# Kernel tuning notes

Hardware: AMD Instinct MI355X
Metric: run time of the kernel (lower is better)

## Reference

```python
import jax, jax.numpy as jnp
import numpy as np

B, N, H, V = 8192, 12, 512, 256  # batch, n_columns, hidden_size, per-column vocab
LN_EPS = 1e-5


def setup_inputs() -> dict:
    key = jax.random.key(0)
    k0, k1, k2, k3 = jax.random.split(key, 4)
    return {
        "input_embedding": jax.random.normal(k0, (B, H), dtype=jnp.float32),
        "features": jax.random.randint(k1, (B, N), 0, V),  # one categorical id per column
        "emb_tables": jax.random.normal(k2, (N, V, H), dtype=jnp.float32) * 0.02,
        "ln_gamma": jnp.ones((2 * H,), dtype=jnp.float32),
        "ln_beta": jnp.zeros((2 * H,), dtype=jnp.float32),
        "pred_W": jax.random.normal(k3, (N, 2 * H, V), dtype=jnp.float32) * 0.02,
        "pred_b": jnp.zeros((N, V), dtype=jnp.float32),
    }


def reference(input_embedding, features, emb_tables, ln_gamma, ln_beta, pred_W, pred_b):
    n = features.shape[1]
    # per-column embedding lookup: emb[b, n] = emb_tables[n, features[b, n]]  -> [B, N, H]
    emb = emb_tables[jnp.arange(n)[None, :], features]
    # _make_masked_sums: triu(diagonal=1) mask summed over dim 1 == exclusive prefix sum
    # over the column axis: masked_sums[b, j] = sum_{i < j} emb[b, i]
    masked_sums = jnp.cumsum(emb, axis=1) - emb  # [B, N, H]
    ctx = jnp.broadcast_to(input_embedding[:, None, :], emb.shape)  # [B, N, H]
    x = jnp.concatenate([ctx, masked_sums], axis=-1)  # [B, N, 2H]
    # LayerNorm over last dim, then exact (erf) GELU as in torch nn.GELU default
    mu = jnp.mean(x, axis=-1, keepdims=True)
    var = jnp.mean(jnp.square(x - mu), axis=-1, keepdims=True)
    xn = (x - mu) * jax.lax.rsqrt(var + LN_EPS) * ln_gamma + ln_beta
    act = jax.nn.gelu(xn, approximate=False)
    # per-column predictor heads: logits[b, n, :] = act[b, n, :] @ pred_W[n] + pred_b[n]
    logits = jnp.einsum('bnh,nhv->bnv', act, pred_W) + pred_b
    return logits
```

## Files before the change

### kernel.cpp

```cpp
#include <hip/hip_runtime.h>
#include <stdint.h>

#define B_SZ 8192
#define N_F 12
#define H_DIM 512
#define K_DIM 1024
#define V_DIM 256

typedef __attribute__((ext_vector_type(8))) __bf16 bf16x8;
typedef __attribute__((ext_vector_type(4))) float f32x4;

__device__ inline float gelu_f(float x) {
  float t = 1.5957691216057308f * x * (1.0f + 0.044715f * x * x);
  return x / (1.0f + __expf(-t));
}

__device__ inline void gld_lds16(const void* g, void* l) {
  __builtin_amdgcn_global_load_lds(
      (const __attribute__((address_space(1))) void*)g,
      (__attribute__((address_space(3))) void*)l, 16, 0, 0);
}

__global__ __launch_bounds__(256, 8) void k_prep(
    const float* __restrict__ ie, const int* __restrict__ feat,
    const float* __restrict__ tab, const float* __restrict__ gam,
    const float* __restrict__ bet, __bf16* actA,
    float* __restrict__ stats) {
  const int lane = threadIdx.x & 63;
  const int b = blockIdx.x * 4 + (threadIdx.x >> 6);

  const float* cb = ie + (size_t)b * H_DIM + lane * 8;
  float4 c0 = *(const float4*)cb;
  float4 c1 = *(const float4*)(cb + 4);
  float s = c0.x + c0.y + c0.z + c0.w + c1.x + c1.y + c1.z + c1.w;
  float q = c0.x * c0.x + c0.y * c0.y + c0.z * c0.z + c0.w * c0.w +
            c1.x * c1.x + c1.y * c1.y + c1.z * c1.z + c1.w * c1.w;
#pragma unroll
  for (int o = 1; o < 64; o <<= 1) {
    s += __shfl_xor(s, o, 64);
    q += __shfl_xor(q, o, 64);
  }
  const float S1 = s, Q1 = q;

  const float4 g0 = *(const float4*)(gam + H_DIM + lane * 8);
  const float4 g1 = *(const float4*)(gam + H_DIM + lane * 8 + 4);
  const float4 e0 = *(const float4*)(bet + H_DIM + lane * 8);
  const float4 e1 = *(const float4*)(bet + H_DIM + lane * 8 + 4);

  float r[8];
#pragma unroll
  for (int i = 0; i < 8; ++i) r[i] = 0.f;

  const int sw = (lane & ~7) | ((lane & 7) ^ (b & 7));
  __bf16* arow = actA + (size_t)b * N_F * H_DIM + sw * 8;

  for (int n = 0; n < N_F; ++n) {
    s = 0.f; q = 0.f;
#pragma unroll
    for (int i = 0; i < 8; ++i) { s += r[i]; q += r[i] * r[i]; }
#pragma unroll
    for (int o = 1; o < 64; o <<= 1) {
      s += __shfl_xor(s, o, 64);
      q += __shfl_xor(q, o, 64);
    }
    const float mean = (S1 + s) * (1.0f / 1024.0f);
    const float var = (Q1 + q) * (1.0f / 1024.0f) - mean * mean;
    const float rs = rsqrtf(var + 1e-5f);
    if (lane == 0)
      *(float2*)(stats + ((size_t)b * N_F + n) * 2) = make_float2(mean, rs);

    float4 t0, t1;
    const bool have = (n < N_F - 1);
    if (have) {
      const int f = feat[b * N_F + n];
      const float* tr = tab + ((size_t)n * V_DIM + f) * H_DIM + lane * 8;
      t0 = *(const float4*)tr;
      t1 = *(const float4*)(tr + 4);
    }

    bf16x8 pk;
    pk[0] = (__bf16)gelu_f((r[0] - mean) * rs * g0.x + e0.x);
    pk[1] = (__bf16)gelu_f((r[1] - mean) * rs * g0.y + e0.y);
    pk[2] = (__bf16)gelu_f((r[2] - mean) * rs * g0.z + e0.z);
    pk[3] = (__bf16)gelu_f((r[3] - mean) * rs * g0.w + e0.w);
    pk[4] = (__bf16)gelu_f((r[4] - mean) * rs * g1.x + e1.x);
    pk[5] = (__bf16)gelu_f((r[5] - mean) * rs * g1.y + e1.y);
    pk[6] = (__bf16)gelu_f((r[6] - mean) * rs * g1.z + e1.z);
    pk[7] = (__bf16)gelu_f((r[7] - mean) * rs * g1.w + e1.w);
    *(bf16x8*)(arow + (size_t)n * H_DIM) = pk;

    if (have) {
      r[0] += t0.x; r[1] += t0.y; r[2] += t0.z; r[3] += t0.w;
      r[4] += t1.x; r[5] += t1.y; r[6] += t1.z; r[7] += t1.w;
    }
  }
}

__global__ __launch_bounds__(256) void k_wt(const float* __restrict__ W,
                                            __bf16* __restrict__ Wt) {
  __shared__ float tile[32][33];
  const int bid = blockIdx.x;
  const int n = bid >> 8;
  const int rem = bid & 255;
  const int kt = rem >> 3, vt = rem & 7;
  const int tx = threadIdx.x & 31, ty = threadIdx.x >> 5;
  const float* src = W + (size_t)n * K_DIM * V_DIM;
#pragma unroll
  for (int i = 0; i < 4; ++i) {
    const int k = kt * 32 + ty + i * 8;
    tile[ty + i * 8][tx] = src[(size_t)k * V_DIM + vt * 32 + tx];
  }
  __syncthreads();
  __bf16* dst = Wt + (size_t)n * V_DIM * K_DIM;
  const int t = threadIdx.x;
  if (t < 128) {
    const int v_l = t >> 2, c_l = t & 3;
    const int v = vt * 32 + v_l;
    bf16x8 pk;
#pragma unroll
    for (int e = 0; e < 8; ++e) pk[e] = (__bf16)tile[c_l * 8 + e][v_l];
    const int gc = kt * 4 + c_l;
    const int swc = (gc & ~7) | ((gc & 7) ^ (v & 7));
    *(bf16x8*)(dst + (size_t)v * K_DIM + swc * 8) = pk;
  }
}

__global__ __launch_bounds__(512, 2) void k_gemm(
    const float* __restrict__ ie, const __bf16* actA,
    const __bf16* __restrict__ Wt, const float* __restrict__ stats,
    const float* __restrict__ gam, const float* __restrict__ bet,
    const float* __restrict__ bias, float* out) {
  constexpr int BM = 128, BN = 256, BK = 64;
  __shared__ __align__(16) __bf16 As[BM * BK];
  __shared__ __align__(16) __bf16 Ws[BN * BK];

  const int n = blockIdx.y;
  const int b0 = blockIdx.x * BM;
  const int t = threadIdx.x;
  const int lane = t & 63;
  const int w = t >> 6;
  const int wm = w & 1;
  const int wn = w >> 1;
  const int l15 = lane & 15;
  const int lq = lane >> 4;
  const int lr8 = lane >> 3;
  const int lo8 = lane & 7;

  const __bf16* Wtn = Wt + (size_t)n * V_DIM * K_DIM;

  const int pr = t >> 3;
  const int pm = t & 7;
  const float2 st0 = *(const float2*)(stats + ((size_t)(b0 + pr) * N_F + n) * 2);
  const float2 st1 =
      *(const float2*)(stats + ((size_t)(b0 + pr + 64) * N_F + n) * 2);

  const int swo = (pm ^ (pr & 7)) << 3;

  bf16x8 ctx[16];

  f32x4 acc[4][4];
#pragma unroll
  for (int i = 0; i < 4; ++i)
#pragma unroll
    for (int j = 0; j < 4; ++j) acc[i][j] = (f32x4){0.f, 0.f, 0.f, 0.f};

#pragma unroll
  for (int kt = 0; kt < 16; ++kt) {
    const int k0p = (kt ^ 8) * BK;
    __syncthreads();
#pragma unroll
    for (int p = 0; p < 4; ++p) {
      const int v0 = w * 32 + p * 8;
      gld_lds16(Wtn + (size_t)(v0 + lr8) * K_DIM + k0p + lo8 * 8, Ws + v0 * BK);
    }
    if (kt < 8) {
#pragma unroll
      for (int p = 0; p < 2; ++p) {
        const int r0 = w * 16 + p * 8;
        gld_lds16(actA + ((size_t)(b0 + r0 + lr8) * N_F + n) * H_DIM +
                      (k0p - H_DIM) + lo8 * 8,
                  As + r0 * BK);
      }
      {
        const int col = kt * 64 + pm * 8;
        const float4 gg0 = *(const float4*)(gam + col);
        const float4 gg1 = *(const float4*)(gam + col + 4);
        const float4 bb0 = *(const float4*)(bet + col);
        const float4 bb1 = *(const float4*)(bet + col + 4);
#pragma unroll
        for (int h = 0; h < 2; ++h) {
          const int row = b0 + pr + 64 * h;
          const float mu = h ? st1.x : st0.x;
          const float rs = h ? st1.y : st0.y;
          const float* ip = ie + (size_t)row * H_DIM + col;
          const float4 x0 = *(const float4*)ip;
          const float4 x1 = *(const float4*)(ip + 4);
          bf16x8 pk;
          pk[0] = (__bf16)gelu_f((x0.x - mu) * rs * gg0.x + bb0.x);
          pk[1] = (__bf16)gelu_f((x0.y - mu) * rs * gg0.y + bb0.y);
          pk[2] = (__bf16)gelu_f((x0.z - mu) * rs * gg0.z + bb0.z);
          pk[3] = (__bf16)gelu_f((x0.w - mu) * rs * gg0.w + bb0.w);
          pk[4] = (__bf16)gelu_f((x1.x - mu) * rs * gg1.x + bb1.x);
          pk[5] = (__bf16)gelu_f((x1.y - mu) * rs * gg1.y + bb1.y);
          pk[6] = (__bf16)gelu_f((x1.z - mu) * rs * gg1.z + bb1.z);
          pk[7] = (__bf16)gelu_f((x1.w - mu) * rs * gg1.w + bb1.w);
          ctx[kt * 2 + h] = pk;
        }
      }
    } else {
      *(bf16x8*)(As + (pr)*BK + swo) = ctx[(kt - 8) * 2 + 0];
      *(bf16x8*)(As + (pr + 64) * BK + swo) = ctx[(kt - 8) * 2 + 1];
    }
    __syncthreads();
#pragma unroll
    for (int ks = 0; ks < 2; ++ks) {
      const int cs = ks * 4 + lq;
      bf16x8 af[4], bb[4];
#pragma unroll
      for (int i = 0; i < 4; ++i) {
        const int row = wm * 64 + i * 16 + l15;
        af[i] = *(const bf16x8*)(As + row * BK + ((cs ^ (row & 7)) << 3));
      }
#pragma unroll
      for (int j = 0; j < 4; ++j) {
        const int row = wn * 64 + j * 16 + l15;
        bb[j] = *(const bf16x8*)(Ws + row * BK + ((cs ^ (row & 7)) << 3));
      }
#pragma unroll
      for (int i = 0; i < 4; ++i)
#pragma unroll
        for (int j = 0; j < 4; ++j)
          acc[i][j] = __builtin_amdgcn_mfma_f32_16x16x32_bf16(af[i], bb[j],
                                                              acc[i][j], 0, 0, 0);
    }
  }

#pragma unroll
  for (int j = 0; j < 4; ++j) {
    const int v = wn * 64 + j * 16 + l15;
    const float bv = bias[n * V_DIM + v];
#pragma unroll
    for (int i = 0; i < 4; ++i) {
      const int rb = wm * 64 + i * 16 + lq * 4;
#pragma unroll
      for (int r = 0; r < 4; ++r) {
        out[((size_t)(b0 + rb + r) * N_F + n) * V_DIM + v] = acc[i][j][r] + bv;
      }
    }
  }
}

extern "C" void kernel_launch(void* const* d_in, const int* in_sizes, int n_in,
                              void* d_out, int out_size, void* d_ws, size_t ws_size,
                              hipStream_t stream) {
  const float* ie = (const float*)d_in[0];
  const int* feat = (const int*)d_in[1];
  const float* tab = (const float*)d_in[2];
  const float* gam = (const float*)d_in[3];
  const float* bet = (const float*)d_in[4];
  const float* predW = (const float*)d_in[5];
  const float* predb = (const float*)d_in[6];
  float* out = (float*)d_out;

  __bf16* actA = (__bf16*)d_out;

  char* ws = (char*)d_ws;
  float* stats = (float*)ws;
  __bf16* Wt = (__bf16*)(ws + 786432);

  hipLaunchKernelGGL(k_prep, dim3(B_SZ / 4), dim3(256), 0, stream, ie, feat,
                     tab, gam, bet, actA, stats);
  hipLaunchKernelGGL(k_wt, dim3(3072), dim3(256), 0, stream, predW, Wt);
  hipLaunchKernelGGL(k_gemm, dim3(B_SZ / 128, N_F), dim3(512), 0, stream, ie,
                     actA, Wt, stats, gam, bet, predb, out);
}
```

Baseline: 269.3 us.

## Stream context activations through double-buffered LDS instead of register-cached precompute

Replaces the 16-entry register cache of precomputed LayerNorm+GELU context fragments with a double-buffered fp32 LDS tile of input_embedding. Each tile is loaded asynchronously with global_load_lds one k-step ahead, and GELU is computed just in time during the second half of the K loop. Gamma and beta are also staged in LDS once per block. The aim is to free VGPRs for occupancy and overlap the ie loads with MMA. The cost is about 64KB of extra LDS per block, which may cap occupancy with 2 blocks of 512 threads, and it relies on the barrier ordering of the async LDS loads being correct.

```diff
diff --git a/kernel.cpp b/kernel.cpp
--- a/kernel.cpp
+++ b/kernel.cpp
@@ -133,6 +133,9 @@
   constexpr int BM = 128, BN = 256, BK = 64;
   __shared__ __align__(16) __bf16 As[BM * BK];
   __shared__ __align__(16) __bf16 Ws[BN * BK];
+  __shared__ __align__(16) float ieS[2][BM * BK];
+  __shared__ __align__(16) float gamS[H_DIM];
+  __shared__ __align__(16) float betS[H_DIM];
 
   const int n = blockIdx.y;
   const int b0 = blockIdx.x * BM;
@@ -148,15 +151,19 @@
 
   const __bf16* Wtn = Wt + (size_t)n * V_DIM * K_DIM;
 
+  if (w == 0) gld_lds16(gam + lane * 4, gamS + lane * 4);
+  else if (w == 1) gld_lds16(gam + 256 + lane * 4, gamS + 256 + lane * 4);
+  else if (w == 2) gld_lds16(bet + lane * 4, betS + lane * 4);
+  else if (w == 3) gld_lds16(bet + 256 + lane * 4, betS + 256 + lane * 4);
+
   const int pr = t >> 3;
   const int pm = t & 7;
   const float2 st0 = *(const float2*)(stats + ((size_t)(b0 + pr) * N_F + n) * 2);
   const float2 st1 =
       *(const float2*)(stats + ((size_t)(b0 + pr + 64) * N_F + n) * 2);
+  asm volatile("" ::"v"(st0.x), "v"(st0.y), "v"(st1.x), "v"(st1.y));
 
   const int swo = (pm ^ (pr & 7)) << 3;
-
-  bf16x8 ctx[16];
 
   f32x4 acc[4][4];
 #pragma unroll
@@ -181,35 +188,54 @@
                       (k0p - H_DIM) + lo8 * 8,
                   As + r0 * BK);
       }
+    } else {
+      const int c = kt - 8;
+      const int col = c * 64 + pm * 8;
+      const float4 gg0 = *(const float4*)(gamS + col);
+      const float4 gg1 = *(const float4*)(gamS + col + 4);
+      const float4 bb0 = *(const float4*)(betS + col);
+      const float4 bb1 = *(const float4*)(betS + col + 4);
+      const float* tile = ieS[c & 1];
       {
-        const int col = kt * 64 + pm * 8;
-        const float4 gg0 = *(const float4*)(gam + col);
-        const float4 gg1 = *(const float4*)(gam + col + 4);
-        const float4 bb0 = *(const float4*)(bet + col);
-        const float4 bb1 = *(const float4*)(bet + col + 4);
-#pragma unroll
-        for (int h = 0; h < 2; ++h) {
-          const int row = b0 + pr + 64 * h;
-          const float mu = h ? st1.x : st0.x;
-          const float rs = h ? st1.y : st0.y;
-          const float* ip = ie + (size_t)row * H_DIM + col;
-          const float4 x0 = *(const float4*)ip;
-          const float4 x1 = *(const float4*)(ip + 4);
-          bf16x8 pk;
-          pk[0] = (__bf16)gelu_f((x0.x - mu) * rs * gg0.x + bb0.x);
-          pk[1] = (__bf16)gelu_f((x0.y - mu) * rs * gg0.y + bb0.y);
-          pk[2] = (__bf16)gelu_f((x0.z - mu) * rs * gg0.z + bb0.z);
-          pk[3] = (__bf16)gelu_f((x0.w - mu) * rs * gg0.w + bb0.w);
-          pk[4] = (__bf16)gelu_f((x1.x - mu) * rs * gg1.x + bb1.x);
-          pk[5] = (__bf16)gelu_f((x1.y - mu) * rs * gg1.y + bb1.y);
-          pk[6] = (__bf16)gelu_f((x1.z - mu) * rs * gg1.z + bb1.z);
-          pk[7] = (__bf16)gelu_f((x1.w - mu) * rs * gg1.w + bb1.w);
-          ctx[kt * 2 + h] = pk;
-        }
-      }
-    } else {
-      *(bf16x8*)(As + (pr)*BK + swo) = ctx[(kt - 8) * 2 + 0];
-      *(bf16x8*)(As + (pr + 64) * BK + swo) = ctx[(kt - 8) * 2 + 1];
+        const float4 x0 = *(const float4*)(tile + pr * 64 + pm * 8);
+        const float4 x1 = *(const float4*)(tile + pr * 64 + pm * 8 + 4);
+        const float mu = st0.x, rs = st0.y;
+        bf16x8 pk;
+        pk[0] = (__bf16)gelu_f((x0.x - mu) * rs * gg0.x + bb0.x);
+        pk[1] = (__bf16)gelu_f((x0.y - mu) * rs * gg0.y + bb0.y);
+        pk[2] = (__bf16)gelu_f((x0.z - mu) * rs * gg0.z + bb0.z);
+        pk[3] = (__bf16)gelu_f((x0.w - mu) * rs * gg0.w + bb0.w);
+        pk[4] = (__bf16)gelu_f((x1.x - mu) * rs * gg1.x + bb1.x);
+        pk[5] = (__bf16)gelu_f((x1.y - mu) * rs * gg1.y + bb1.y);
+        pk[6] = (__bf16)gelu_f((x1.z - mu) * rs * gg1.z + bb1.z);
+        pk[7] = (__bf16)gelu_f((x1.w - mu) * rs * gg1.w + bb1.w);
+        *(bf16x8*)(As + pr * BK + swo) = pk;
+      }
+      {
+        const float4 x0 = *(const float4*)(tile + (pr + 64) * 64 + pm * 8);
+        const float4 x1 = *(const float4*)(tile + (pr + 64) * 64 + pm * 8 + 4);
+        const float mu = st1.x, rs = st1.y;
+        bf16x8 pk;
+        pk[0] = (__bf16)gelu_f((x0.x - mu) * rs * gg0.x + bb0.x);
+        pk[1] = (__bf16)gelu_f((x0.y - mu) * rs * gg0.y + bb0.y);
+        pk[2] = (__bf16)gelu_f((x0.z - mu) * rs * gg0.z + bb0.z);
+        pk[3] = (__bf16)gelu_f((x0.w - mu) * rs * gg0.w + bb0.w);
+        pk[4] = (__bf16)gelu_f((x1.x - mu) * rs * gg1.x + bb1.x);
+        pk[5] = (__bf16)gelu_f((x1.y - mu) * rs * gg1.y + bb1.y);
+        pk[6] = (__bf16)gelu_f((x1.z - mu) * rs * gg1.z + bb1.z);
+        pk[7] = (__bf16)gelu_f((x1.w - mu) * rs * gg1.w + bb1.w);
+        *(bf16x8*)(As + (pr + 64) * BK + swo) = pk;
+      }
+    }
+    if (kt >= 7 && kt < 15) {
+      const int c = kt - 7;
+      float* dst = ieS[c & 1];
+#pragma unroll
+      for (int i = 0; i < 4; ++i) {
+        const int c4 = i * 512 + t;
+        gld_lds16(ie + (size_t)(b0 + (c4 >> 4)) * H_DIM + c * 64 + (c4 & 15) * 4,
+                  dst + c4 * 4);
+      }
     }
     __syncthreads();
 #pragma unroll
```

After: 268.5 us. Within noise of the previous version (-0.3%).
